# Optimization experiments

Measured on AMD Instinct MI355X. Metric: run time of the kernel, lower is better.

Reference implementation:

```python
import jax, jax.numpy as jnp
import numpy as np

B, S, F = 4, 2048, 8
D, H, L, FF = 256, 8, 2, 1024
DH = D // H
NSK, NPAT = 2000, 64
DQ = D // 4  # pattern/feat sub-embedding width


def setup_inputs() -> dict:
    key = jax.random.key(0)
    ks = jax.random.split(key, 32)
    r = lambda i, shape: jax.random.normal(ks[i], shape, jnp.float32) * 0.02
    return {
        'interactions': jax.random.randint(ks[0], (B, S), 0, 2 * NSK),
        'patterns': jax.random.randint(ks[1], (B, S), 0, NPAT),
        'forget_features': jax.random.normal(ks[2], (B, S, F), jnp.float32),
        'inter_emb': r(3, (2 * NSK, D)),
        'pattern_emb': r(4, (NPAT, DQ)),
        'feat_W': r(5, (F, DQ)), 'feat_b': jnp.zeros((DQ,), jnp.float32),
        'in_W': r(6, (D + 2 * DQ, D)), 'in_b': jnp.zeros((D,), jnp.float32),
        'time_W': r(7, (1, D)), 'time_b': jnp.zeros((D,), jnp.float32),
        'pos_W': r(8, (1, D)), 'pos_b': jnp.zeros((D,), jnp.float32),
        'Wq': r(9, (L, D, H, DH)), 'bq': jnp.zeros((L, H, DH), jnp.float32),
        'Wk': r(10, (L, D, H, DH)), 'bk': jnp.zeros((L, H, DH), jnp.float32),
        'Wv': r(11, (L, D, H, DH)), 'bv': jnp.zeros((L, H, DH), jnp.float32),
        'Wo': r(12, (L, H, DH, D)), 'bo': jnp.zeros((L, D), jnp.float32),
        'kerple_p': jnp.full((L, H, 1, 1), 0.5, jnp.float32),
        'kerple_a': jnp.zeros((L, H, 1, 1), jnp.float32),
        'ln1_g': jnp.ones((L, D), jnp.float32), 'ln1_b': jnp.zeros((L, D), jnp.float32),
        'ln2_g': jnp.ones((L, D), jnp.float32), 'ln2_b': jnp.zeros((L, D), jnp.float32),
        'ffn_W1': r(13, (L, D, FF)), 'ffn_b1': jnp.zeros((L, FF), jnp.float32),
        'ffn_W2': r(14, (L, FF, D)), 'ffn_b2': jnp.zeros((L, D), jnp.float32),
        'out_W': r(15, (D, NSK)), 'out_b': jnp.zeros((NSK,), jnp.float32),
    }


def _ln(x, g, b, eps=1e-6):
    m = jnp.mean(x, -1, keepdims=True)
    v = jnp.mean(jnp.square(x - m), -1, keepdims=True)
    return g * (x - m) * jax.lax.rsqrt(v + eps) + b


def reference(interactions, patterns, forget_features, inter_emb, pattern_emb,
              feat_W, feat_b, in_W, in_b, time_W, time_b, pos_W, pos_b,
              Wq, bq, Wk, bk, Wv, bv, Wo, bo, kerple_p, kerple_a,
              ln1_g, ln1_b, ln2_g, ln2_b, ffn_W1, ffn_b1, ffn_W2, ffn_b2,
              out_W, out_b):
    inter_e = inter_emb[interactions]                      # [B,S,D]
    pat_e = pattern_emb[patterns]                          # [B,S,D/4]
    feat_e = forget_features @ feat_W + feat_b             # [B,S,D/4]
    x = jnp.concatenate([inter_e, pat_e, feat_e], -1) @ in_W + in_b  # [B,S,D]
    elapsed = forget_features[:, :, 0:1]
    time_enc = jnp.tanh(elapsed @ time_W + time_b)
    pos = jnp.arange(S, dtype=jnp.float32)[None, :, None] / jnp.float32(S)
    pos_enc = pos @ pos_W + pos_b
    x = x + time_enc + pos_enc

    positions = jnp.arange(S, dtype=jnp.float32)
    dist = jnp.maximum(positions[:, None] - positions[None, :], 0.0)  # [S,S]
    causal_bias = jnp.triu(jnp.full((S, S), -1e9, jnp.float32), 1)    # [S,S]
    inv_sqrt_dh = 1.0 / jnp.sqrt(jnp.float32(DH))

    for i in range(L):
        p = jax.nn.softplus(kerple_p[i])                   # [H,1,1]
        a = jax.nn.softplus(kerple_a[i])
        bias = causal_bias[None] - p * jnp.log1p(a * dist[None])  # [H,S,S]
        q = jnp.einsum('bsd,dhk->bshk', x, Wq[i]) + bq[i]
        k = jnp.einsum('bsd,dhk->bshk', x, Wk[i]) + bk[i]
        v = jnp.einsum('bsd,dhk->bshk', x, Wv[i]) + bv[i]
        scores = jnp.einsum('bshk,bthk->bhst', q, k) * inv_sqrt_dh + bias[None]
        attn = jax.nn.softmax(scores, axis=-1)
        o = jnp.einsum('bhst,bthk->bshk', attn, v)
        attn_out = jnp.einsum('bshk,hkd->bsd', o, Wo[i]) + bo[i]
        x = _ln(x + attn_out, ln1_g[i], ln1_b[i])
        h = jax.nn.gelu(x @ ffn_W1[i] + ffn_b1[i], approximate=False)
        ffn_out = h @ ffn_W2[i] + ffn_b2[i]
        x = _ln(x + ffn_out, ln2_g[i], ln2_b[i])
    return x @ out_W + out_b
```

## Files before the change

### kernel.cpp

```cpp
#include <hip/hip_runtime.h>
#include <math.h>

#define SEQ   2048
#define BATCH 4
#define NTOK  8192
#define DM    256
#define NHD   8
#define DHD   32
#define DFF   1024
#define NSKC  2000

typedef __attribute__((ext_vector_type(8))) short short8;
typedef __attribute__((ext_vector_type(4))) float f32x4;
typedef unsigned short ushort_t;

#define QPRE ((float)(0.17677669529663687 * 1.4426950408889634))

__device__ __forceinline__ ushort_t f2bf(float x) {
    union { float f; unsigned u; } c; c.f = x;
    unsigned r = c.u + 0x7FFFu + ((c.u >> 16) & 1u);
    return (ushort_t)(r >> 16);
}

struct ConvSeg { const float* src; ushort_t* dst; int K; int N; int Npad; };
struct ConvArgs { ConvSeg s[14]; };

__global__ __launch_bounds__(256) void convert_kernel(ConvArgs args) {
    ConvSeg sg = args.s[blockIdx.z];
    int n0 = blockIdx.x * 32, k0 = blockIdx.y * 32;
    if (n0 >= sg.Npad || k0 >= sg.K) return;
    __shared__ float T[32][33];
    int tid = threadIdx.x;
    int tn = tid & 31, tk4 = tid >> 5;
#pragma unroll
    for (int i = 0; i < 4; i++) {
        int kl = tk4 + i * 8;
        float v = 0.0f;
        if (n0 + tn < sg.N) v = sg.src[(size_t)(k0 + kl) * sg.N + n0 + tn];
        T[kl][tn] = v;
    }
    __syncthreads();
    int tk = tid & 31, tn4 = tid >> 5;
#pragma unroll
    for (int i = 0; i < 4; i++) {
        int nl = tn4 + i * 8;
        sg.dst[(size_t)(n0 + nl) * sg.K + k0 + tk] = f2bf(T[tk][nl]);
    }
}

__global__ __launch_bounds__(384) void concat_kernel(
    const int* __restrict__ interactions, const int* __restrict__ patterns,
    const float* __restrict__ ff, const float* __restrict__ inter_emb,
    const float* __restrict__ pattern_emb, const float* __restrict__ feat_W,
    const float* __restrict__ feat_b, ushort_t* __restrict__ out)
{
    int tok = blockIdx.x;
    int j = threadIdx.x;
    float v;
    if (j < 256) {
        v = inter_emb[(size_t)interactions[tok] * 256 + j];
    } else if (j < 320) {
        v = pattern_emb[patterns[tok] * 64 + (j - 256)];
    } else {
        int c = j - 320;
        float acc = feat_b[c];
#pragma unroll
        for (int f = 0; f < 8; f++) acc += ff[tok * 8 + f] * feat_W[f * 64 + c];
        v = acc;
    }
    out[(size_t)tok * 384 + j] = f2bf(v);
}

__global__ __launch_bounds__(256) void addenc_kernel(
    float* __restrict__ x, ushort_t* __restrict__ xb, const float* __restrict__ ff,
    const float* __restrict__ time_W, const float* __restrict__ time_b,
    const float* __restrict__ pos_W, const float* __restrict__ pos_b)
{
    int tok = blockIdx.x;
    int d = threadIdx.x;
    int s = tok & (SEQ - 1);
    float el = ff[tok * 8];
    float te = tanhf(el * time_W[d] + time_b[d]);
    float pe = ((float)s * (1.0f / (float)SEQ)) * pos_W[d] + pos_b[d];
    size_t idx = (size_t)tok * DM + d;
    float nv = x[idx] + te + pe;
    x[idx] = nv;
    xb[idx] = f2bf(nv);
}

__global__ __launch_bounds__(256) void ln_kernel(
    float* __restrict__ x, const float* __restrict__ r,
    const float* __restrict__ g, const float* __restrict__ b,
    ushort_t* __restrict__ xb)
{
    int tok = blockIdx.x;
    int d = threadIdx.x;
    size_t idx = (size_t)tok * DM + d;
    float v = x[idx] + r[idx];
    float s1 = v, s2 = v * v;
#pragma unroll
    for (int off = 32; off > 0; off >>= 1) {
        s1 += __shfl_down(s1, off, 64);
        s2 += __shfl_down(s2, off, 64);
    }
    __shared__ float red1[4], red2[4];
    int wid = d >> 6, lane = d & 63;
    if (lane == 0) { red1[wid] = s1; red2[wid] = s2; }
    __syncthreads();
    s1 = red1[0] + red1[1] + red1[2] + red1[3];
    s2 = red2[0] + red2[1] + red2[2] + red2[3];
    float mean = s1 * (1.0f / 256.0f);
    float var = s2 * (1.0f / 256.0f) - mean * mean;
    float inv = rsqrtf(var + 1e-6f);
    float nv = g[d] * (v - mean) * inv + b[d];
    x[idx] = nv;
    xb[idx] = f2bf(nv);
}

__global__ __launch_bounds__(256) void gemm_bf16(
    const ushort_t* __restrict__ A, const ushort_t* __restrict__ Bt,
    int M, int N, int K,
    float* __restrict__ Cf, const float* __restrict__ b0)
{
    __shared__ ushort_t As[128][40];
    __shared__ ushort_t Bs[64][40];
    int m0 = blockIdx.y * 128, n0 = blockIdx.x * 64;
    int tid = threadIdx.x;
    int wv = tid >> 6, lane = tid & 63;
    int quad = lane >> 4, l16 = lane & 15;
    int srow = tid >> 2, sc = (tid & 3) << 3;

    f32x4 acc[2][4];
#pragma unroll
    for (int i = 0; i < 2; i++)
#pragma unroll
        for (int j = 0; j < 4; j++) acc[i][j] = (f32x4){0.f, 0.f, 0.f, 0.f};

    uint4 pa0 = *(const uint4*)&A[(size_t)(m0 + srow) * K + sc];
    uint4 pa1 = *(const uint4*)&A[(size_t)(m0 + 64 + srow) * K + sc];
    uint4 pbb = *(const uint4*)&Bt[(size_t)(n0 + srow) * K + sc];

    int msub = wv * 32;
    for (int k0 = 0; k0 < K; k0 += 32) {
        __syncthreads();
        *(uint4*)&As[srow][sc] = pa0;
        *(uint4*)&As[64 + srow][sc] = pa1;
        *(uint4*)&Bs[srow][sc] = pbb;
        __syncthreads();
        if (k0 + 32 < K) {
            pa0 = *(const uint4*)&A[(size_t)(m0 + srow) * K + k0 + 32 + sc];
            pa1 = *(const uint4*)&A[(size_t)(m0 + 64 + srow) * K + k0 + 32 + sc];
            pbb = *(const uint4*)&Bt[(size_t)(n0 + srow) * K + k0 + 32 + sc];
        }
        short8 af0 = *(const short8*)&As[msub + l16][quad * 8];
        short8 af1 = *(const short8*)&As[msub + 16 + l16][quad * 8];
        short8 bf0 = *(const short8*)&Bs[l16][quad * 8];
        short8 bf1 = *(const short8*)&Bs[16 + l16][quad * 8];
        short8 bf2 = *(const short8*)&Bs[32 + l16][quad * 8];
        short8 bf3 = *(const short8*)&Bs[48 + l16][quad * 8];
        acc[0][0] = __builtin_amdgcn_mfma_f32_16x16x32_bf16(af0, bf0, acc[0][0], 0, 0, 0);
        acc[0][1] = __builtin_amdgcn_mfma_f32_16x16x32_bf16(af0, bf1, acc[0][1], 0, 0, 0);
        acc[0][2] = __builtin_amdgcn_mfma_f32_16x16x32_bf16(af0, bf2, acc[0][2], 0, 0, 0);
        acc[0][3] = __builtin_amdgcn_mfma_f32_16x16x32_bf16(af0, bf3, acc[0][3], 0, 0, 0);
        acc[1][0] = __builtin_amdgcn_mfma_f32_16x16x32_bf16(af1, bf0, acc[1][0], 0, 0, 0);
        acc[1][1] = __builtin_amdgcn_mfma_f32_16x16x32_bf16(af1, bf1, acc[1][1], 0, 0, 0);
        acc[1][2] = __builtin_amdgcn_mfma_f32_16x16x32_bf16(af1, bf2, acc[1][2], 0, 0, 0);
        acc[1][3] = __builtin_amdgcn_mfma_f32_16x16x32_bf16(af1, bf3, acc[1][3], 0, 0, 0);
    }

#pragma unroll
    for (int mt = 0; mt < 2; mt++) {
#pragma unroll
        for (int nt = 0; nt < 4; nt++) {
            int n = n0 + nt * 16 + l16;
#pragma unroll
            for (int r = 0; r < 4; r++) {
                int m = m0 + msub + mt * 16 + quad * 4 + r;
                Cf[(size_t)m * N + n] = acc[mt][nt][r] + b0[n];
            }
        }
    }
}

__global__ __launch_bounds__(256) void gemm_bf16_128(
    const ushort_t* __restrict__ A, const ushort_t* __restrict__ Bt,
    int M, int N, int K, int mode,
    float* __restrict__ Cf, ushort_t* __restrict__ Cb,
    ushort_t* __restrict__ Ck, ushort_t* __restrict__ Cv,
    const float* __restrict__ b0, const float* __restrict__ b1,
    const float* __restrict__ b2, int Nreal)
{
    __shared__ ushort_t As[128][40];
    __shared__ ushort_t Bs[128][40];
    int m0 = blockIdx.y * 128, n0 = blockIdx.x * 128;
    int tid = threadIdx.x;
    int wv = tid >> 6, lane = tid & 63;
    int quad = lane >> 4, l16 = lane & 15;
    int wm = (wv >> 1) * 64, wn = (wv & 1) * 64;
    int srow = tid >> 1, sc = (tid & 1) << 4;

    f32x4 acc[4][4];
#pragma unroll
    for (int i = 0; i < 4; i++)
#pragma unroll
        for (int j = 0; j < 4; j++) acc[i][j] = (f32x4){0.f, 0.f, 0.f, 0.f};

    uint4 pa0 = *(const uint4*)&A[(size_t)(m0 + srow) * K + sc];
    uint4 pa1 = *(const uint4*)&A[(size_t)(m0 + srow) * K + sc + 8];
    uint4 pb0 = *(const uint4*)&Bt[(size_t)(n0 + srow) * K + sc];
    uint4 pb1 = *(const uint4*)&Bt[(size_t)(n0 + srow) * K + sc + 8];

    for (int k0 = 0; k0 < K; k0 += 32) {
        __syncthreads();
        *(uint4*)&As[srow][sc] = pa0;
        *(uint4*)&As[srow][sc + 8] = pa1;
        *(uint4*)&Bs[srow][sc] = pb0;
        *(uint4*)&Bs[srow][sc + 8] = pb1;
        __syncthreads();
        if (k0 + 32 < K) {
            pa0 = *(const uint4*)&A[(size_t)(m0 + srow) * K + k0 + 32 + sc];
            pa1 = *(const uint4*)&A[(size_t)(m0 + srow) * K + k0 + 32 + sc + 8];
            pb0 = *(const uint4*)&Bt[(size_t)(n0 + srow) * K + k0 + 32 + sc];
            pb1 = *(const uint4*)&Bt[(size_t)(n0 + srow) * K + k0 + 32 + sc + 8];
        }
        short8 af[4], bf[4];
#pragma unroll
        for (int i = 0; i < 4; i++) {
            af[i] = *(const short8*)&As[wm + i * 16 + l16][quad * 8];
            bf[i] = *(const short8*)&Bs[wn + i * 16 + l16][quad * 8];
        }
#pragma unroll
        for (int i = 0; i < 4; i++)
#pragma unroll
            for (int j = 0; j < 4; j++)
                acc[i][j] = __builtin_amdgcn_mfma_f32_16x16x32_bf16(af[i], bf[j], acc[i][j], 0, 0, 0);
    }

#pragma unroll
    for (int i = 0; i < 4; i++) {
#pragma unroll
        for (int j = 0; j < 4; j++) {
            int n = n0 + wn + j * 16 + l16;
#pragma unroll
            for (int r = 0; r < 4; r++) {
                int m = m0 + wm + i * 16 + quad * 4 + r;
                float v = acc[i][j][r];
                if (mode == 1) {
                    float t = v + b0[n];
                    t = 0.5f * t * (1.0f + erff(t * 0.70710678118654752f));
                    Cb[(size_t)m * N + n] = f2bf(t);
                } else if (mode == 3) {
                    if (n < Nreal) Cf[(size_t)m * Nreal + n] = v + b0[n];
                } else {
                    int which = n >> 8, idx = n & 255;
                    int hh = idx >> 5, d = idx & 31;
                    int s = m & (SEQ - 1), b = m >> 11;
                    if (which == 0)
                        Cb[(((size_t)(b * NHD + hh)) * SEQ + s) * DHD + d] =
                            f2bf((v + b0[idx]) * QPRE);
                    else if (which == 1)
                        Ck[(((size_t)(b * NHD + hh)) * SEQ + s) * DHD + d] = f2bf(v + b1[idx]);
                    else {
                        int sp = (s & ~31) | (((s & 15) << 1) | ((s >> 4) & 1));
                        Cv[(((size_t)(b * NHD + hh)) * DHD + d) * SEQ + sp] = f2bf(v + b2[idx]);
                    }
                }
            }
        }
    }
}

__global__ __launch_bounds__(256) void attn_mfma(
    const ushort_t* __restrict__ qb, const ushort_t* __restrict__ kb,
    const ushort_t* __restrict__ vtb, const float* __restrict__ kp,
    const float* __restrict__ ka, ushort_t* __restrict__ ob)
{
    int h = blockIdx.y, b = blockIdx.z;
    int tid = threadIdx.x, wv = tid >> 6, lane = tid & 63;
    int quad = lane >> 4, l16 = lane & 15;
    __shared__ ushort_t P2[4][2][16 * 40];

    float p = log1pf(__expf(kp[h]));
    float a = log1pf(__expf(ka[h]));

    int bh = b * NHD + h;
    const ushort_t* Qh = qb + (size_t)bh * SEQ * DHD;
    const ushort_t* Kh = kb + (size_t)bh * SEQ * DHD;
    const ushort_t* Vh = vtb + (size_t)bh * DHD * SEQ;

    int j = blockIdx.x * 4 + wv;
    int tlo = j, thi = 127 - j;
    int qlo0 = tlo * 16, qhi0 = thi * 16;

    short8 qfl = *(const short8*)&Qh[(qlo0 + l16) * DHD + quad * 8];
    short8 qfh = *(const short8*)&Qh[(qhi0 + l16) * DHD + quad * 8];
    f32x4 ol0 = (f32x4){0.f,0.f,0.f,0.f}, ol1 = (f32x4){0.f,0.f,0.f,0.f};
    f32x4 oh0 = (f32x4){0.f,0.f,0.f,0.f}, oh1 = (f32x4){0.f,0.f,0.f,0.f};
    float lsl[4] = {0.f,0.f,0.f,0.f}, lsh[4] = {0.f,0.f,0.f,0.f};
    ushort_t* Pl = &P2[wv][0][0];
    ushort_t* Ph = &P2[wv][1][0];

    int nch_hi = (thi + 2) >> 1;
    int nch_lo = (tlo + 2) >> 1;
    int qsrh = qhi0 + quad * 4;
    int qsrl = qlo0 + quad * 4;

    for (int ch = 0; ch < nch_hi; ch++) {
        int k0 = ch * 32;
        short8 kf0 = *(const short8*)&Kh[(k0 + l16) * DHD + quad * 8];
        short8 kf1 = *(const short8*)&Kh[(k0 + 16 + l16) * DHD + quad * 8];
        short8 vf0 = *(const short8*)&Vh[l16 * SEQ + k0 + quad * 8];
        short8 vf1 = *(const short8*)&Vh[(16 + l16) * SEQ + k0 + quad * 8];
        f32x4 z = (f32x4){0.f,0.f,0.f,0.f};

        f32x4 s0 = __builtin_amdgcn_mfma_f32_16x16x32_bf16(qfh, kf0, z, 0, 0, 0);
        f32x4 s1 = __builtin_amdgcn_mfma_f32_16x16x32_bf16(qfh, kf1, z, 0, 0, 0);
        {
            float df = (float)(qsrh - k0 - l16);
            bool interior = (k0 + 31 <= qhi0);
#pragma unroll
            for (int r = 0; r < 4; r++) {
                float d0 = df + (float)r, d1 = d0 - 16.0f;
                float e0 = exp2f(s0[r] - p * __log2f(fmaf(a, d0, 1.0f)));
                float e1 = exp2f(s1[r] - p * __log2f(fmaf(a, d1, 1.0f)));
                if (!interior) {
                    e0 = (d0 >= 0.0f) ? e0 : 0.0f;
                    e1 = (d1 >= 0.0f) ? e1 : 0.0f;
                }
                lsh[r] += e0 + e1;
                unsigned pk = (unsigned)f2bf(e0) | ((unsigned)f2bf(e1) << 16);
                *(unsigned*)&Ph[(quad * 4 + r) * 40 + l16 * 2] = pk;
            }
        }

        bool do_lo = (ch < nch_lo);
        if (do_lo) {
            f32x4 t0 = __builtin_amdgcn_mfma_f32_16x16x32_bf16(qfl, kf0, z, 0, 0, 0);
            f32x4 t1 = __builtin_amdgcn_mfma_f32_16x16x32_bf16(qfl, kf1, z, 0, 0, 0);
            float df = (float)(qsrl - k0 - l16);
            bool interior = (k0 + 31 <= qlo0);
#pragma unroll
            for (int r = 0; r < 4; r++) {
                float d0 = df + (float)r, d1 = d0 - 16.0f;
                float e0 = exp2f(t0[r] - p * __log2f(fmaf(a, d0, 1.0f)));
                float e1 = exp2f(t1[r] - p * __log2f(fmaf(a, d1, 1.0f)));
                if (!interior) {
                    e0 = (d0 >= 0.0f) ? e0 : 0.0f;
                    e1 = (d1 >= 0.0f) ? e1 : 0.0f;
                }
                lsl[r] += e0 + e1;
                unsigned pk = (unsigned)f2bf(e0) | ((unsigned)f2bf(e1) << 16);
                *(unsigned*)&Pl[(quad * 4 + r) * 40 + l16 * 2] = pk;
            }
        }

        __builtin_amdgcn_s_waitcnt(0xC07F);
        __builtin_amdgcn_wave_barrier();
        short8 pfh = *(const short8*)&Ph[l16 * 40 + quad * 8];
        oh0 = __builtin_amdgcn_mfma_f32_16x16x32_bf16(pfh, vf0, oh0, 0, 0, 0);
        oh1 = __builtin_amdgcn_mfma_f32_16x16x32_bf16(pfh, vf1, oh1, 0, 0, 0);
        if (do_lo) {
            short8 pfl = *(const short8*)&Pl[l16 * 40 + quad * 8];
            ol0 = __builtin_amdgcn_mfma_f32_16x16x32_bf16(pfl, vf0, ol0, 0, 0, 0);
            ol1 = __builtin_amdgcn_mfma_f32_16x16x32_bf16(pfl, vf1, ol1, 0, 0, 0);
        }
    }

#pragma unroll
    for (int r = 0; r < 4; r++) {
#pragma unroll
        for (int off = 1; off < 16; off <<= 1) {
            lsh[r] += __shfl_xor(lsh[r], off, 16);
            lsl[r] += __shfl_xor(lsl[r], off, 16);
        }
    }
#pragma unroll
    for (int r = 0; r < 4; r++) {
        float rh = 1.0f / lsh[r];
        float rl = 1.0f / lsl[r];
        size_t bh_ = ((size_t)(b * SEQ + qsrh + r)) * DM + h * DHD;
        size_t bl_ = ((size_t)(b * SEQ + qsrl + r)) * DM + h * DHD;
        ob[bh_ + l16]      = f2bf(oh0[r] * rh);
        ob[bh_ + 16 + l16] = f2bf(oh1[r] * rh);
        ob[bl_ + l16]      = f2bf(ol0[r] * rl);
        ob[bl_ + 16 + l16] = f2bf(ol1[r] * rl);
    }
}

extern "C" void kernel_launch(void* const* d_in, const int* in_sizes, int n_in,
                              void* d_out, int out_size, void* d_ws, size_t ws_size,
                              hipStream_t stream) {
    const int*   interactions = (const int*)d_in[0];
    const int*   patterns     = (const int*)d_in[1];
    const float* ff           = (const float*)d_in[2];
    const float* inter_emb    = (const float*)d_in[3];
    const float* pattern_emb  = (const float*)d_in[4];
    const float* feat_W       = (const float*)d_in[5];
    const float* feat_b       = (const float*)d_in[6];
    const float* in_W         = (const float*)d_in[7];
    const float* in_b         = (const float*)d_in[8];
    const float* time_W       = (const float*)d_in[9];
    const float* time_b       = (const float*)d_in[10];
    const float* pos_W        = (const float*)d_in[11];
    const float* pos_b        = (const float*)d_in[12];
    const float* Wq           = (const float*)d_in[13];
    const float* bq           = (const float*)d_in[14];
    const float* Wk           = (const float*)d_in[15];
    const float* bk           = (const float*)d_in[16];
    const float* Wv           = (const float*)d_in[17];
    const float* bv           = (const float*)d_in[18];
    const float* Wo           = (const float*)d_in[19];
    const float* bo           = (const float*)d_in[20];
    const float* kerple_p     = (const float*)d_in[21];
    const float* kerple_a     = (const float*)d_in[22];
    const float* ln1_g        = (const float*)d_in[23];
    const float* ln1_b        = (const float*)d_in[24];
    const float* ln2_g        = (const float*)d_in[25];
    const float* ln2_b        = (const float*)d_in[26];
    const float* ffn_W1       = (const float*)d_in[27];
    const float* ffn_b1       = (const float*)d_in[28];
    const float* ffn_W2       = (const float*)d_in[29];
    const float* ffn_b2       = (const float*)d_in[30];
    const float* out_W        = (const float*)d_in[31];
    const float* out_b        = (const float*)d_in[32];
    float* out = (float*)d_out;

    char* wsb = (char*)d_ws;
    const size_t MB = 1024 * 1024;
    float*    x    = (float*)(wsb + 0);
    float*    tmp  = (float*)(wsb + 8  * MB);
    ushort_t* xb   = (ushort_t*)(wsb + 16 * MB);
    ushort_t* qbuf = (ushort_t*)(wsb + 20 * MB);
    ushort_t* kbuf = (ushort_t*)(wsb + 24 * MB);
    ushort_t* vtbf = (ushort_t*)(wsb + 28 * MB);
    ushort_t* shrd = (ushort_t*)(wsb + 32 * MB);
    ushort_t* cbuf = shrd;
    ushort_t* o_bf = shrd;
    ushort_t* h_bf = shrd;
    char* wp = wsb + 48 * MB;
    ushort_t* inWt  = (ushort_t*)wp;  wp += 256  * 384 * 2;
    ushort_t* qkvWt = (ushort_t*)wp;  wp += 2 * 768 * 256 * 2;
    ushort_t* WoT   = (ushort_t*)wp;  wp += 2 * 256 * 256 * 2;
    ushort_t* W1T   = (ushort_t*)wp;  wp += 2 * 1024 * 256 * 2;
    ushort_t* W2T   = (ushort_t*)wp;  wp += 2 * 256 * 1024 * 2;
    ushort_t* outWt = (ushort_t*)wp;  wp += 2048 * 256 * 2;

    ConvArgs ca;
    int D2 = 256 * 256;
    ca.s[0]  = { in_W,              inWt,               384,  256,  256 };
    ca.s[1]  = { Wq,                qkvWt,              256,  256,  256 };
    ca.s[2]  = { Wk,                qkvWt + 1 * D2,     256,  256,  256 };
    ca.s[3]  = { Wv,                qkvWt + 2 * D2,     256,  256,  256 };
    ca.s[4]  = { Wq + D2,           qkvWt + 3 * D2,     256,  256,  256 };
    ca.s[5]  = { Wk + D2,           qkvWt + 4 * D2,     256,  256,  256 };
    ca.s[6]  = { Wv + D2,           qkvWt + 5 * D2,     256,  256,  256 };
    ca.s[7]  = { Wo,                WoT,                256,  256,  256 };
    ca.s[8]  = { Wo + D2,           WoT + D2,           256,  256,  256 };
    ca.s[9]  = { ffn_W1,            W1T,                256,  1024, 1024 };
    ca.s[10] = { ffn_W1 + 4 * D2,   W1T + 4 * D2,       256,  1024, 1024 };
    ca.s[11] = { ffn_W2,            W2T,                1024, 256,  256 };
    ca.s[12] = { ffn_W2 + 4 * D2,   W2T + 4 * D2,       1024, 256,  256 };
    ca.s[13] = { out_W,             outWt,              256,  2000, 2048 };
    convert_kernel<<<dim3(64, 32, 14), 256, 0, stream>>>(ca);

    concat_kernel<<<NTOK, 384, 0, stream>>>(interactions, patterns, ff,
                                            inter_emb, pattern_emb, feat_W, feat_b, cbuf);
    gemm_bf16<<<dim3(4, 64), 256, 0, stream>>>(cbuf, inWt, NTOK, 256, 384, x, in_b);
    addenc_kernel<<<NTOK, 256, 0, stream>>>(x, xb, ff, time_W, time_b, pos_W, pos_b);

    for (int l = 0; l < 2; l++) {
        gemm_bf16_128<<<dim3(6, 64), 256, 0, stream>>>(
            xb, qkvWt + (size_t)l * 768 * 256, NTOK, 768, 256, 2,
            nullptr, qbuf, kbuf, vtbf,
            bq + l * 256, bk + l * 256, bv + l * 256, 0);
        attn_mfma<<<dim3(16, NHD, BATCH), 256, 0, stream>>>(
            qbuf, kbuf, vtbf, kerple_p + l * NHD, kerple_a + l * NHD, o_bf);
        gemm_bf16<<<dim3(4, 64), 256, 0, stream>>>(
            o_bf, WoT + (size_t)l * D2, NTOK, 256, 256, tmp, bo + l * 256);
        ln_kernel<<<NTOK, 256, 0, stream>>>(x, tmp, ln1_g + l * 256, ln1_b + l * 256, xb);
        gemm_bf16_128<<<dim3(8, 64), 256, 0, stream>>>(
            xb, W1T + (size_t)l * 4 * D2, NTOK, 1024, 256, 1,
            nullptr, h_bf, nullptr, nullptr, ffn_b1 + l * 1024, nullptr, nullptr, 0);
        gemm_bf16<<<dim3(4, 64), 256, 0, stream>>>(
            h_bf, W2T + (size_t)l * 4 * D2, NTOK, 256, 1024, tmp, ffn_b2 + l * 256);
        ln_kernel<<<NTOK, 256, 0, stream>>>(x, tmp, ln2_g + l * 256, ln2_b + l * 256, xb);
    }

    gemm_bf16_128<<<dim3(16, 64), 256, 0, stream>>>(
        xb, outWt, NTOK, 2048, 256, 3,
        out, nullptr, nullptr, nullptr, out_b, nullptr, nullptr, NSKC);
}
```

Baseline: 488.7 us.

## Table-driven KERPLE bias, split-K attention waves, fused encoding GEMM, bf16 residual temps

Attention now precomputes the KERPLE distance-decay weights into a shared-memory table, which also zeroes the non-causal entries. Each query-tile pair is split across two waves that handle alternating key chunks and are merged through shared memory, and the grid is doubled. The input projection GEMM absorbs the time and position encoding, replacing a separate kernel. The N=256 GEMMs use 64-row tiles and write bf16 residuals that the layernorm reads, and the weight conversion launch is compacted into a 1-D grid. The changes cut transcendental work and launch count and raise occupancy, at the cost of an extra block barrier in attention and lower precision in the residual branch.

```diff
diff --git a/kernel.cpp b/kernel.cpp
--- a/kernel.cpp
+++ b/kernel.cpp
@@ -22,13 +22,37 @@
     return (ushort_t)(r >> 16);
 }
 
-struct ConvSeg { const float* src; ushort_t* dst; int K; int N; int Npad; };
+#if __has_builtin(__builtin_amdgcn_cvt_pk_bf16_f32)
+typedef __attribute__((ext_vector_type(2))) __bf16 bf16x2_t;
+__device__ __forceinline__ unsigned pack_bf16(float a, float b) {
+    bf16x2_t r = __builtin_amdgcn_cvt_pk_bf16_f32(a, b);
+    union { bf16x2_t v; unsigned u; } c; c.v = r;
+    return c.u;
+}
+#else
+__device__ __forceinline__ unsigned pack_bf16(float a, float b) {
+    return (unsigned)f2bf(a) | ((unsigned)f2bf(b) << 16);
+}
+#endif
+
+__device__ __forceinline__ float bf2f(ushort_t x) {
+    union { unsigned u; float f; } c; c.u = ((unsigned)x) << 16;
+    return c.f;
+}
+
+struct ConvSeg { const float* src; ushort_t* dst; int K; int N; int ntx; int base; };
 struct ConvArgs { ConvSeg s[14]; };
 
 __global__ __launch_bounds__(256) void convert_kernel(ConvArgs args) {
-    ConvSeg sg = args.s[blockIdx.z];
-    int n0 = blockIdx.x * 32, k0 = blockIdx.y * 32;
-    if (n0 >= sg.Npad || k0 >= sg.K) return;
+    int bid = blockIdx.x;
+    int si = 0;
+#pragma unroll
+    for (int i = 1; i < 14; i++) if (bid >= args.s[i].base) si = i;
+    ConvSeg sg = args.s[si];
+    int local = bid - sg.base;
+    int ty = local / sg.ntx;
+    int tx = local - ty * sg.ntx;
+    int n0 = tx * 32, k0 = ty * 32;
     __shared__ float T[32][33];
     int tid = threadIdx.x;
     int tn = tid & 31, tk4 = tid >> 5;
@@ -71,32 +95,15 @@
     out[(size_t)tok * 384 + j] = f2bf(v);
 }
 
-__global__ __launch_bounds__(256) void addenc_kernel(
-    float* __restrict__ x, ushort_t* __restrict__ xb, const float* __restrict__ ff,
-    const float* __restrict__ time_W, const float* __restrict__ time_b,
-    const float* __restrict__ pos_W, const float* __restrict__ pos_b)
-{
-    int tok = blockIdx.x;
-    int d = threadIdx.x;
-    int s = tok & (SEQ - 1);
-    float el = ff[tok * 8];
-    float te = tanhf(el * time_W[d] + time_b[d]);
-    float pe = ((float)s * (1.0f / (float)SEQ)) * pos_W[d] + pos_b[d];
-    size_t idx = (size_t)tok * DM + d;
-    float nv = x[idx] + te + pe;
-    x[idx] = nv;
-    xb[idx] = f2bf(nv);
-}
-
 __global__ __launch_bounds__(256) void ln_kernel(
-    float* __restrict__ x, const float* __restrict__ r,
+    float* __restrict__ x, const ushort_t* __restrict__ r,
     const float* __restrict__ g, const float* __restrict__ b,
     ushort_t* __restrict__ xb)
 {
     int tok = blockIdx.x;
     int d = threadIdx.x;
     size_t idx = (size_t)tok * DM + d;
-    float v = x[idx] + r[idx];
+    float v = x[idx] + bf2f(r[idx]);
     float s1 = v, s2 = v * v;
 #pragma unroll
     for (int off = 32; off > 0; off >>= 1) {
@@ -117,66 +124,72 @@
     xb[idx] = f2bf(nv);
 }
 
-__global__ __launch_bounds__(256) void gemm_bf16(
+__global__ __launch_bounds__(256) void gemm64(
     const ushort_t* __restrict__ A, const ushort_t* __restrict__ Bt,
-    int M, int N, int K,
-    float* __restrict__ Cf, const float* __restrict__ b0)
+    int M, int N, int K, int mode,
+    float* __restrict__ Cf, ushort_t* __restrict__ Cb,
+    const float* __restrict__ b0,
+    const float* __restrict__ ffg, const float* __restrict__ tW,
+    const float* __restrict__ tb, const float* __restrict__ pW,
+    const float* __restrict__ pb)
 {
-    __shared__ ushort_t As[128][40];
+    __shared__ ushort_t As[64][40];
     __shared__ ushort_t Bs[64][40];
-    int m0 = blockIdx.y * 128, n0 = blockIdx.x * 64;
+    int m0 = blockIdx.y * 64, n0 = blockIdx.x * 64;
     int tid = threadIdx.x;
     int wv = tid >> 6, lane = tid & 63;
     int quad = lane >> 4, l16 = lane & 15;
     int srow = tid >> 2, sc = (tid & 3) << 3;
 
-    f32x4 acc[2][4];
-#pragma unroll
-    for (int i = 0; i < 2; i++)
-#pragma unroll
-        for (int j = 0; j < 4; j++) acc[i][j] = (f32x4){0.f, 0.f, 0.f, 0.f};
-
-    uint4 pa0 = *(const uint4*)&A[(size_t)(m0 + srow) * K + sc];
-    uint4 pa1 = *(const uint4*)&A[(size_t)(m0 + 64 + srow) * K + sc];
-    uint4 pbb = *(const uint4*)&Bt[(size_t)(n0 + srow) * K + sc];
-
-    int msub = wv * 32;
+    f32x4 acc[4];
+#pragma unroll
+    for (int j = 0; j < 4; j++) acc[j] = (f32x4){0.f, 0.f, 0.f, 0.f};
+
+    uint4 pa = *(const uint4*)&A[(size_t)(m0 + srow) * K + sc];
+    uint4 pbv = *(const uint4*)&Bt[(size_t)(n0 + srow) * K + sc];
+
+    int mrow = wv * 16;
     for (int k0 = 0; k0 < K; k0 += 32) {
         __syncthreads();
-        *(uint4*)&As[srow][sc] = pa0;
-        *(uint4*)&As[64 + srow][sc] = pa1;
-        *(uint4*)&Bs[srow][sc] = pbb;
+        *(uint4*)&As[srow][sc] = pa;
+        *(uint4*)&Bs[srow][sc] = pbv;
         __syncthreads();
         if (k0 + 32 < K) {
-            pa0 = *(const uint4*)&A[(size_t)(m0 + srow) * K + k0 + 32 + sc];
-            pa1 = *(const uint4*)&A[(size_t)(m0 + 64 + srow) * K + k0 + 32 + sc];
-            pbb = *(const uint4*)&Bt[(size_t)(n0 + srow) * K + k0 + 32 + sc];
-        }
-        short8 af0 = *(const short8*)&As[msub + l16][quad * 8];
-        short8 af1 = *(const short8*)&As[msub + 16 + l16][quad * 8];
+            pa = *(const uint4*)&A[(size_t)(m0 + srow) * K + k0 + 32 + sc];
+            pbv = *(const uint4*)&Bt[(size_t)(n0 + srow) * K + k0 + 32 + sc];
+        }
+        short8 af = *(const short8*)&As[mrow + l16][quad * 8];
         short8 bf0 = *(const short8*)&Bs[l16][quad * 8];
         short8 bf1 = *(const short8*)&Bs[16 + l16][quad * 8];
         short8 bf2 = *(const short8*)&Bs[32 + l16][quad * 8];
         short8 bf3 = *(const short8*)&Bs[48 + l16][quad * 8];
-        acc[0][0] = __builtin_amdgcn_mfma_f32_16x16x32_bf16(af0, bf0, acc[0][0], 0, 0, 0);
-        acc[0][1] = __builtin_amdgcn_mfma_f32_16x16x32_bf16(af0, bf1, acc[0][1], 0, 0, 0);
-        acc[0][2] = __builtin_amdgcn_mfma_f32_16x16x32_bf16(af0, bf2, acc[0][2], 0, 0, 0);
-        acc[0][3] = __builtin_amdgcn_mfma_f32_16x16x32_bf16(af0, bf3, acc[0][3], 0, 0, 0);
-        acc[1][0] = __builtin_amdgcn_mfma_f32_16x16x32_bf16(af1, bf0, acc[1][0], 0, 0, 0);
-        acc[1][1] = __builtin_amdgcn_mfma_f32_16x16x32_bf16(af1, bf1, acc[1][1], 0, 0, 0);
-        acc[1][2] = __builtin_amdgcn_mfma_f32_16x16x32_bf16(af1, bf2, acc[1][2], 0, 0, 0);
-        acc[1][3] = __builtin_amdgcn_mfma_f32_16x16x32_bf16(af1, bf3, acc[1][3], 0, 0, 0);
-    }
-
-#pragma unroll
-    for (int mt = 0; mt < 2; mt++) {
-#pragma unroll
-        for (int nt = 0; nt < 4; nt++) {
-            int n = n0 + nt * 16 + l16;
-#pragma unroll
-            for (int r = 0; r < 4; r++) {
-                int m = m0 + msub + mt * 16 + quad * 4 + r;
-                Cf[(size_t)m * N + n] = acc[mt][nt][r] + b0[n];
+        acc[0] = __builtin_amdgcn_mfma_f32_16x16x32_bf16(af, bf0, acc[0], 0, 0, 0);
+        acc[1] = __builtin_amdgcn_mfma_f32_16x16x32_bf16(af, bf1, acc[1], 0, 0, 0);
+        acc[2] = __builtin_amdgcn_mfma_f32_16x16x32_bf16(af, bf2, acc[2], 0, 0, 0);
+        acc[3] = __builtin_amdgcn_mfma_f32_16x16x32_bf16(af, bf3, acc[3], 0, 0, 0);
+    }
+
+#pragma unroll
+    for (int r = 0; r < 4; r++) {
+        int m = m0 + mrow + quad * 4 + r;
+        if (mode == 4) {
+            int s = m & (SEQ - 1);
+            float el = ffg[m * 8];
+            float pos = (float)s * (1.0f / (float)SEQ);
+#pragma unroll
+            for (int nt = 0; nt < 4; nt++) {
+                int n = n0 + nt * 16 + l16;
+                float te = tanhf(el * tW[n] + tb[n]);
+                float pe = pos * pW[n] + pb[n];
+                float nv = acc[nt][r] + b0[n] + te + pe;
+                Cf[(size_t)m * N + n] = nv;
+                Cb[(size_t)m * N + n] = f2bf(nv);
+            }
+        } else {
+#pragma unroll
+            for (int nt = 0; nt < 4; nt++) {
+                int n = n0 + nt * 16 + l16;
+                Cb[(size_t)m * N + n] = f2bf(acc[nt][r] + b0[n]);
             }
         }
     }
@@ -278,18 +291,28 @@
     int h = blockIdx.y, b = blockIdx.z;
     int tid = threadIdx.x, wv = tid >> 6, lane = tid & 63;
     int quad = lane >> 4, l16 = lane & 15;
+    int pair = wv >> 1, parity = wv & 1;
+
+    __shared__ float tabs[2112];
     __shared__ ushort_t P2[4][2][16 * 40];
+    __shared__ float Cmb[2][64][28];
 
     float p = log1pf(__expf(kp[h]));
     float a = log1pf(__expf(ka[h]));
+    for (int i = tid; i < 2112; i += 256) {
+        float w = 0.0f;
+        if (i >= 64) w = exp2f(-p * __log2f(fmaf(a, (float)(i - 64), 1.0f)));
+        tabs[i] = w;
+    }
+    __syncthreads();
 
     int bh = b * NHD + h;
     const ushort_t* Qh = qb + (size_t)bh * SEQ * DHD;
     const ushort_t* Kh = kb + (size_t)bh * SEQ * DHD;
     const ushort_t* Vh = vtb + (size_t)bh * DHD * SEQ;
 
-    int j = blockIdx.x * 4 + wv;
-    int tlo = j, thi = 127 - j;
+    int pj = blockIdx.x * 2 + pair;
+    int tlo = pj, thi = 127 - pj;
     int qlo0 = tlo * 16, qhi0 = thi * 16;
 
     short8 qfl = *(const short8*)&Qh[(qlo0 + l16) * DHD + quad * 8];
@@ -305,7 +328,7 @@
     int qsrh = qhi0 + quad * 4;
     int qsrl = qlo0 + quad * 4;
 
-    for (int ch = 0; ch < nch_hi; ch++) {
+    for (int ch = parity; ch < nch_hi; ch += 2) {
         int k0 = ch * 32;
         short8 kf0 = *(const short8*)&Kh[(k0 + l16) * DHD + quad * 8];
         short8 kf1 = *(const short8*)&Kh[(k0 + 16 + l16) * DHD + quad * 8];
@@ -316,45 +339,29 @@
         f32x4 s0 = __builtin_amdgcn_mfma_f32_16x16x32_bf16(qfh, kf0, z, 0, 0, 0);
         f32x4 s1 = __builtin_amdgcn_mfma_f32_16x16x32_bf16(qfh, kf1, z, 0, 0, 0);
         {
-            float df = (float)(qsrh - k0 - l16);
-            bool interior = (k0 + 31 <= qhi0);
+            const float* tp = &tabs[qsrh - k0 - l16 + 48];
 #pragma unroll
             for (int r = 0; r < 4; r++) {
-                float d0 = df + (float)r, d1 = d0 - 16.0f;
-                float e0 = exp2f(s0[r] - p * __log2f(fmaf(a, d0, 1.0f)));
-                float e1 = exp2f(s1[r] - p * __log2f(fmaf(a, d1, 1.0f)));
-                if (!interior) {
-                    e0 = (d0 >= 0.0f) ? e0 : 0.0f;
-                    e1 = (d1 >= 0.0f) ? e1 : 0.0f;
-                }
+                float e0 = exp2f(s0[r]) * tp[16 + r];
+                float e1 = exp2f(s1[r]) * tp[r];
                 lsh[r] += e0 + e1;
-                unsigned pk = (unsigned)f2bf(e0) | ((unsigned)f2bf(e1) << 16);
-                *(unsigned*)&Ph[(quad * 4 + r) * 40 + l16 * 2] = pk;
+                *(unsigned*)&Ph[(quad * 4 + r) * 40 + l16 * 2] = pack_bf16(e0, e1);
             }
         }
-
         bool do_lo = (ch < nch_lo);
         if (do_lo) {
             f32x4 t0 = __builtin_amdgcn_mfma_f32_16x16x32_bf16(qfl, kf0, z, 0, 0, 0);
             f32x4 t1 = __builtin_amdgcn_mfma_f32_16x16x32_bf16(qfl, kf1, z, 0, 0, 0);
-            float df = (float)(qsrl - k0 - l16);
-            bool interior = (k0 + 31 <= qlo0);
+            const float* tq = &tabs[qsrl - k0 - l16 + 48];
 #pragma unroll
             for (int r = 0; r < 4; r++) {
-                float d0 = df + (float)r, d1 = d0 - 16.0f;
-                float e0 = exp2f(t0[r] - p * __log2f(fmaf(a, d0, 1.0f)));
-                float e1 = exp2f(t1[r] - p * __log2f(fmaf(a, d1, 1.0f)));
-                if (!interior) {
-                    e0 = (d0 >= 0.0f) ? e0 : 0.0f;
-                    e1 = (d1 >= 0.0f) ? e1 : 0.0f;
-                }
+                float e0 = exp2f(t0[r]) * tq[16 + r];
+                float e1 = exp2f(t1[r]) * tq[r];
                 lsl[r] += e0 + e1;
-                unsigned pk = (unsigned)f2bf(e0) | ((unsigned)f2bf(e1) << 16);
-                *(unsigned*)&Pl[(quad * 4 + r) * 40 + l16 * 2] = pk;
+                *(unsigned*)&Pl[(quad * 4 + r) * 40 + l16 * 2] = pack_bf16(e0, e1);
             }
         }
 
-        __builtin_amdgcn_s_waitcnt(0xC07F);
         __builtin_amdgcn_wave_barrier();
         short8 pfh = *(const short8*)&Ph[l16 * 40 + quad * 8];
         oh0 = __builtin_amdgcn_mfma_f32_16x16x32_bf16(pfh, vf0, oh0, 0, 0, 0);
@@ -366,24 +373,43 @@
         }
     }
 
-#pragma unroll
-    for (int r = 0; r < 4; r++) {
-#pragma unroll
-        for (int off = 1; off < 16; off <<= 1) {
-            lsh[r] += __shfl_xor(lsh[r], off, 16);
-            lsl[r] += __shfl_xor(lsl[r], off, 16);
-        }
-    }
-#pragma unroll
-    for (int r = 0; r < 4; r++) {
-        float rh = 1.0f / lsh[r];
-        float rl = 1.0f / lsl[r];
-        size_t bh_ = ((size_t)(b * SEQ + qsrh + r)) * DM + h * DHD;
-        size_t bl_ = ((size_t)(b * SEQ + qsrl + r)) * DM + h * DHD;
-        ob[bh_ + l16]      = f2bf(oh0[r] * rh);
-        ob[bh_ + 16 + l16] = f2bf(oh1[r] * rh);
-        ob[bl_ + l16]      = f2bf(ol0[r] * rl);
-        ob[bl_ + 16 + l16] = f2bf(ol1[r] * rl);
+    if (parity == 1) {
+        float* cp = &Cmb[pair][lane][0];
+        *(float4*)&cp[0]  = (float4){oh0[0], oh0[1], oh0[2], oh0[3]};
+        *(float4*)&cp[4]  = (float4){oh1[0], oh1[1], oh1[2], oh1[3]};
+        *(float4*)&cp[8]  = (float4){ol0[0], ol0[1], ol0[2], ol0[3]};
+        *(float4*)&cp[12] = (float4){ol1[0], ol1[1], ol1[2], ol1[3]};
+        *(float4*)&cp[16] = (float4){lsh[0], lsh[1], lsh[2], lsh[3]};
+        *(float4*)&cp[20] = (float4){lsl[0], lsl[1], lsl[2], lsl[3]};
+    }
+    __syncthreads();
+    if (parity == 0) {
+        const float* cp = &Cmb[pair][lane][0];
+#pragma unroll
+        for (int i = 0; i < 4; i++) {
+            oh0[i] += cp[i];      oh1[i] += cp[4 + i];
+            ol0[i] += cp[8 + i];  ol1[i] += cp[12 + i];
+            lsh[i] += cp[16 + i]; lsl[i] += cp[20 + i];
+        }
+#pragma unroll
+        for (int r = 0; r < 4; r++) {
+#pragma unroll
+            for (int off = 1; off < 16; off <<= 1) {
+                lsh[r] += __shfl_xor(lsh[r], off, 16);
+                lsl[r] += __shfl_xor(lsl[r], off, 16);
+            }
+        }
+#pragma unroll
+        for (int r = 0; r < 4; r++) {
+            float rh = 1.0f / lsh[r];
+            float rl = 1.0f / lsl[r];
+            size_t bh_ = ((size_t)(b * SEQ + qsrh + r)) * DM + h * DHD;
+            size_t bl_ = ((size_t)(b * SEQ + qsrl + r)) * DM + h * DHD;
+            ob[bh_ + l16]      = f2bf(oh0[r] * rh);
+            ob[bh_ + 16 + l16] = f2bf(oh1[r] * rh);
+            ob[bl_ + l16]      = f2bf(ol0[r] * rl);
+            ob[bl_ + 16 + l16] = f2bf(ol1[r] * rl);
+        }
     }
 }
 
@@ -428,7 +454,7 @@
     char* wsb = (char*)d_ws;
     const size_t MB = 1024 * 1024;
     float*    x    = (float*)(wsb + 0);
-    float*    tmp  = (float*)(wsb + 8  * MB);
+    ushort_t* tmpb = (ushort_t*)(wsb + 8  * MB);
     ushort_t* xb   = (ushort_t*)(wsb + 16 * MB);
     ushort_t* qbuf = (ushort_t*)(wsb + 20 * MB);
     ushort_t* kbuf = (ushort_t*)(wsb + 24 * MB);
@@ -447,43 +473,51 @@
 
     ConvArgs ca;
     int D2 = 256 * 256;
-    ca.s[0]  = { in_W,              inWt,               384,  256,  256 };
-    ca.s[1]  = { Wq,                qkvWt,              256,  256,  256 };
-    ca.s[2]  = { Wk,                qkvWt + 1 * D2,     256,  256,  256 };
-    ca.s[3]  = { Wv,                qkvWt + 2 * D2,     256,  256,  256 };
-    ca.s[4]  = { Wq + D2,           qkvWt + 3 * D2,     256,  256,  256 };
-    ca.s[5]  = { Wk + D2,           qkvWt + 4 * D2,     256,  256,  256 };
-    ca.s[6]  = { Wv + D2,           qkvWt + 5 * D2,     256,  256,  256 };
-    ca.s[7]  = { Wo,                WoT,                256,  256,  256 };
-    ca.s[8]  = { Wo + D2,           WoT + D2,           256,  256,  256 };
-    ca.s[9]  = { ffn_W1,            W1T,                256,  1024, 1024 };
-    ca.s[10] = { ffn_W1 + 4 * D2,   W1T + 4 * D2,       256,  1024, 1024 };
-    ca.s[11] = { ffn_W2,            W2T,                1024, 256,  256 };
-    ca.s[12] = { ffn_W2 + 4 * D2,   W2T + 4 * D2,       1024, 256,  256 };
-    ca.s[13] = { out_W,             outWt,              256,  2000, 2048 };
-    convert_kernel<<<dim3(64, 32, 14), 256, 0, stream>>>(ca);
+    int base = 0, ib = 0;
+    auto addseg = [&](const float* src, ushort_t* dst, int K, int N, int Npad) {
+        ca.s[ib].src = src; ca.s[ib].dst = dst; ca.s[ib].K = K; ca.s[ib].N = N;
+        ca.s[ib].ntx = Npad / 32; ca.s[ib].base = base;
+        base += (Npad / 32) * (K / 32); ib++;
+    };
+    addseg(in_W,            inWt,           384,  256,  256);
+    addseg(Wq,              qkvWt,          256,  256,  256);
+    addseg(Wk,              qkvWt + 1 * D2, 256,  256,  256);
+    addseg(Wv,              qkvWt + 2 * D2, 256,  256,  256);
+    addseg(Wq + D2,         qkvWt + 3 * D2, 256,  256,  256);
+    addseg(Wk + D2,         qkvWt + 4 * D2, 256,  256,  256);
+    addseg(Wv + D2,         qkvWt + 5 * D2, 256,  256,  256);
+    addseg(Wo,              WoT,            256,  256,  256);
+    addseg(Wo + D2,         WoT + D2,       256,  256,  256);
+    addseg(ffn_W1,          W1T,            256,  1024, 1024);
+    addseg(ffn_W1 + 4 * D2, W1T + 4 * D2,   256,  1024, 1024);
+    addseg(ffn_W2,          W2T,            1024, 256,  256);
+    addseg(ffn_W2 + 4 * D2, W2T + 4 * D2,   1024, 256,  256);
+    addseg(out_W,           outWt,          256,  2000, 2048);
+    convert_kernel<<<base, 256, 0, stream>>>(ca);
 
     concat_kernel<<<NTOK, 384, 0, stream>>>(interactions, patterns, ff,
                                             inter_emb, pattern_emb, feat_W, feat_b, cbuf);
-    gemm_bf16<<<dim3(4, 64), 256, 0, stream>>>(cbuf, inWt, NTOK, 256, 384, x, in_b);
-    addenc_kernel<<<NTOK, 256, 0, stream>>>(x, xb, ff, time_W, time_b, pos_W, pos_b);
+    gemm64<<<dim3(4, 128), 256, 0, stream>>>(cbuf, inWt, NTOK, 256, 384, 4,
+                                             x, xb, in_b, ff, time_W, time_b, pos_W, pos_b);
 
     for (int l = 0; l < 2; l++) {
         gemm_bf16_128<<<dim3(6, 64), 256, 0, stream>>>(
             xb, qkvWt + (size_t)l * 768 * 256, NTOK, 768, 256, 2,
             nullptr, qbuf, kbuf, vtbf,
             bq + l * 256, bk + l * 256, bv + l * 256, 0);
-        attn_mfma<<<dim3(16, NHD, BATCH), 256, 0, stream>>>(
+        attn_mfma<<<dim3(32, NHD, BATCH), 256, 0, stream>>>(
             qbuf, kbuf, vtbf, kerple_p + l * NHD, kerple_a + l * NHD, o_bf);
-        gemm_bf16<<<dim3(4, 64), 256, 0, stream>>>(
-            o_bf, WoT + (size_t)l * D2, NTOK, 256, 256, tmp, bo + l * 256);
-        ln_kernel<<<NTOK, 256, 0, stream>>>(x, tmp, ln1_g + l * 256, ln1_b + l * 256, xb);
+        gemm64<<<dim3(4, 128), 256, 0, stream>>>(
+            o_bf, WoT + (size_t)l * D2, NTOK, 256, 256, 5,
+            nullptr, tmpb, bo + l * 256, nullptr, nullptr, nullptr, nullptr, nullptr);
+        ln_kernel<<<NTOK, 256, 0, stream>>>(x, tmpb, ln1_g + l * 256, ln1_b + l * 256, xb);
         gemm_bf16_128<<<dim3(8, 64), 256, 0, stream>>>(
             xb, W1T + (size_t)l * 4 * D2, NTOK, 1024, 256, 1,
             nullptr, h_bf, nullptr, nullptr, ffn_b1 + l * 1024, nullptr, nullptr, 0);
-        gemm_bf16<<<dim3(4, 64), 256, 0, stream>>>(
-            h_bf, W2T + (size_t)l * 4 * D2, NTOK, 256, 1024, tmp, ffn_b2 + l * 256);
-        ln_kernel<<<NTOK, 256, 0, stream>>>(x, tmp, ln2_g + l * 256, ln2_b + l * 256, xb);
+        gemm64<<<dim3(4, 128), 256, 0, stream>>>(
+            h_bf, W2T + (size_t)l * 4 * D2, NTOK, 256, 1024, 5,
+            nullptr, tmpb, ffn_b2 + l * 256, nullptr, nullptr, nullptr, nullptr, nullptr);
+        ln_kernel<<<NTOK, 256, 0, stream>>>(x, tmpb, ln2_g + l * 256, ln2_b + l * 256, xb);
     }
 
     gemm_bf16_128<<<dim3(16, 64), 256, 0, stream>>>(
```

Result: no change. 483.1 us (-1.1%).
